# Kernel tuning notes

Hardware: AMD Instinct MI355X
Metric: run time of the kernel (lower is better)

The kernel has to match this reference:

```python
import jax, jax.numpy as jnp
import numpy as np

WS = 32          # window_size (== k passed to rounding helper)
R = 4            # num_relations
H = 8            # num_heads
D = 64           # out_features (head dim)
FIN = 256        # in_features
LENGTHS = [251, 247, 263, 255, 240, 258, 249, 260, 252, 245, 256, 250, 248, 261, 244, 254]


def _statics(lengths, ws):
    """Static index bookkeeping mirroring round_up_to_nearest_k_and_a_window_size,
    insert_zero_rows and the post-hoc index removal in forward()."""
    l = np.asarray(lengths, dtype=np.int64)
    tgt = (l + ws - 1) // ws * ws + ws            # per-graph padded length (+1 extra window)
    starts = np.concatenate([[0], np.cumsum(tgt)[:-1]])
    pad_even = starts - np.arange(len(l)) * ws + l  # padding start in trimmed frame
    pad_odd_win = (starts + tgt - ws) // ws         # window index of each extra padding window
    L = int(tgt.sum())
    w = L // ws
    # positions of real nodes inside the padded sequence
    pos = np.concatenate([s + np.arange(n) for s, n in zip(starts, l)])
    extra = set(pad_odd_win.tolist())
    rem_windows = np.array([i for i in range(w) if i not in extra], dtype=np.int64)
    Wp = len(rem_windows)
    removed = set()
    for p in pad_even:
        nm = (int(p) + ws - 1) // ws * ws
        removed.update(range(int(p), nm))
    rem_final = np.array([i for i in range(Wp * ws) if i not in removed], dtype=np.int64)
    return L, w, pos, rem_windows, rem_final


def setup_inputs() -> dict:
    key = jax.random.key(0)
    k1, k2, k3, k4, k5 = jax.random.split(key, 5)
    N = int(sum(LENGTHS))
    node_features = jax.random.normal(k1, (R, N, FIN), dtype=jnp.float32)
    Wq = jax.random.normal(k2, (H * D, FIN), dtype=jnp.float32) * 0.02
    b_q = jax.random.normal(k3, (H * D,), dtype=jnp.float32) * 0.02
    Wk = jax.random.normal(k4, (H * D, FIN), dtype=jnp.float32) * 0.02
    b_k = jax.random.normal(k5, (H * D,), dtype=jnp.float32) * 0.02
    num_nodes = jnp.asarray(LENGTHS, dtype=jnp.int64)
    return {"node_features": node_features, "Wq": Wq, "b_q": b_q, "Wk": Wk, "b_k": b_k,
            "num_nodes": num_nodes}


def reference(node_features, Wq, b_q, Wk, b_k, num_nodes):
    lengths = np.asarray(num_nodes).tolist()
    L, w, pos, rem_w, rem_f = _statics(lengths, WS)
    Rr, N, Fi = node_features.shape

    # insert_zero_rows: scatter real nodes into padded [R, L, F]; bool key mask [L]
    padded = jnp.zeros((Rr, L, Fi), node_features.dtype).at[:, pos].set(node_features)
    maskL = np.zeros(L, dtype=bool)
    maskL[pos] = True

    # Q/K projections -> [R*H, L, D]
    Q = (padded @ Wq.T + b_q).reshape(Rr, L, H, D).transpose(0, 2, 1, 3).reshape(Rr * H, L, D)
    K = (padded @ Wk.T + b_k).reshape(Rr, L, H, D).transpose(0, 2, 1, 3).reshape(Rr * H, L, D)

    scale = D ** -0.5
    qb = Q.reshape(-1, w, WS, D) * scale            # [B, w, ws, D]
    kb = K.reshape(-1, w, WS, D)
    # look_around keys (backward=1, forward=1, pad_value=-1)
    pk = jnp.pad(kb, ((0, 0), (1, 1), (0, 0), (0, 0)), constant_values=-1.0)
    k3 = jnp.concatenate([pk[:, i:i + w] for i in range(3)], axis=2)  # [B, w, 3ws, D]

    # static validity mask: key-position pad mask AND look-around of real-node mask
    t = np.arange(L).reshape(w, WS)
    pt = np.pad(t, ((1, 1), (0, 0)), constant_values=-1)
    t3 = np.concatenate([pt[i:i + w] for i in range(3)], axis=1)      # [w, 3ws]
    mw = maskL.reshape(w, WS)
    pm = np.pad(mw, ((1, 1), (0, 0)), constant_values=False)
    m3 = np.concatenate([pm[i:i + w] for i in range(3)], axis=1)      # [w, 3ws]
    valid = jnp.asarray(m3 & (t3 != -1))[None, :, None, :]            # [1, w, 1, 3ws]

    sim = jnp.einsum('bwid,bwjd->bwij', qb, k3)                        # [B, w, ws, 3ws]
    NEG = -jnp.finfo(sim.dtype).max
    sim = jnp.where(valid, sim, NEG)

    # drop pure-padding extra windows, softmax (dropout omitted: eval mode)
    attn = jax.nn.softmax(sim[:, rem_w], axis=-1)                      # [B, Wp, ws, 3ws]
    Wp = rem_w.shape[0]
    score = attn.reshape(Rr, H, Wp, WS, 3 * WS).mean(axis=1)           # [R, Wp, ws, 3ws]

    # displace blocks to banded rectangle, then trim first/last window of columns
    wi = np.arange(Wp)[:, None, None]
    ri = np.arange(WS)[None, :, None]
    ci = (np.arange(Wp) * WS)[:, None, None] + np.arange(3 * WS)[None, None, :]
    full = jnp.zeros((Rr, Wp, WS, (Wp + 2) * WS), score.dtype)
    full = full.at[:, wi, ri, ci].set(score)
    rect = full.reshape(Rr, Wp * WS, (Wp + 2) * WS)[:, :, WS:-WS]      # [R, Wp*ws, Wp*ws]

    # remove intra-window padding rows and columns
    rect = rect[:, rem_f][:, :, rem_f]                                 # [R, N, N]
    n = rem_f.shape[0]
    return rect.transpose(1, 0, 2).reshape(n, Rr * n)                  # [N, R*N]
```

## Files before the change

### kernel.cpp

```cpp
#include <hip/hip_runtime.h>
#include <stdint.h>

typedef float f32x4 __attribute__((ext_vector_type(4)));
typedef short s16x8 __attribute__((ext_vector_type(8)));
typedef unsigned short u16x4 __attribute__((ext_vector_type(4)));
typedef unsigned short u16x8 __attribute__((ext_vector_type(8)));

#define NG 16
__constant__ int c_LEN[NG]   = {251,247,263,255,240,258,249,260,252,245,256,250,248,261,244,254};
__constant__ int c_CUM[NG+1] = {0,251,498,761,1016,1256,1514,1763,2023,2275,2520,2776,3026,3274,3535,3779,4033};
__constant__ int c_KWC[NG+1] = {0,8,16,25,33,41,50,58,67,75,83,91,99,107,116,124,132};

#define NTOT 4033
#define RN   16132
#define NWIN 132
#define NEGF (-3.0e38f)

#define ZS 2304
#define ZCHUNKA 9292032L
#define ZBLOCKS 2024
#define AZB 264

#define OFF_WB 8259584
#define OFF_QK 8783872

__device__ __forceinline__ unsigned short f2bf(float f){
  union { float f; uint32_t u; } x; x.f = f;
  uint32_t u = x.u;
  u += 0x7fffu + ((u >> 16) & 1u);
  return (unsigned short)(u >> 16);
}

__device__ __forceinline__ f32x4 mfma16(s16x8 a, s16x8 b, f32x4 c){
  return __builtin_amdgcn_mfma_f32_16x16x32_bf16(a, b, c, 0, 0, 0);
}

#define NX4  1032448
#define NWQ4 32768
#define NCV4 1097984
__global__ void convert_kernel(const float* __restrict__ X,
                               const float* __restrict__ Wq,
                               const float* __restrict__ Wk,
                               unsigned short* __restrict__ Xb,
                               unsigned short* __restrict__ Wb){
  int i = blockIdx.x * 256 + threadIdx.x;
  if (i >= NCV4) return;
  const float* src; unsigned short* dst;
  if (i < NX4){ src = X + (size_t)i * 4; dst = Xb + (size_t)i * 4; }
  else {
    int k = i - NX4;
    if (k < NWQ4){ src = Wq + (size_t)k * 4; dst = Wb + (size_t)k * 4; }
    else         { src = Wk + (size_t)(k - NWQ4) * 4; dst = Wb + (size_t)k * 4; }
  }
  f32x4 v = *(const f32x4*)src;
  u16x4 o;
  #pragma unroll
  for (int c = 0; c < 4; ++c) o[c] = f2bf(v[c]);
  *(u16x4*)dst = o;
}

#define LP 68
__global__ __launch_bounds__(256) void projzero_kernel(const unsigned short* __restrict__ Xb,
                                                       const unsigned short* __restrict__ Wb,
                                                       const float* __restrict__ bq,
                                                       const float* __restrict__ bk,
                                                       unsigned short* __restrict__ QK,
                                                       float* __restrict__ out){
  __shared__ float tile[64 * LP];

  int bid = blockIdx.x;
  int grp = bid / 3;
  int rem = bid - grp * 3;

  if (rem == 2){
    f32x4 z = {0.f, 0.f, 0.f, 0.f};
    f32x4* o4 = (f32x4*)out;
    long stride = (long)ZBLOCKS * 256;
    for (long i = (long)grp * 256 + threadIdx.x; i < ZCHUNKA; i += stride)
      o4[i] = z;
    return;
  }

  int pi = grp * 2 + rem;
  int col0 = (pi & 15) * 64;
  int row0 = (pi >> 4) * 64;

  int tid  = threadIdx.x;
  int lane = tid & 63, wid = tid >> 6;
  int l15  = lane & 15, quad = lane >> 4;
  int wm = wid & 1, wn = wid >> 1;
  int rowW = row0 + wm * 32;
  int colW = col0 + wn * 32;

  f32x4 acc[2][2];
  #pragma unroll
  for (int m = 0; m < 2; ++m)
    #pragma unroll
    for (int n = 0; n < 2; ++n){ acc[m][n][0]=0.f; acc[m][n][1]=0.f; acc[m][n][2]=0.f; acc[m][n][3]=0.f; }

  int r0 = min(rowW + l15,      RN - 1);
  int r1 = min(rowW + 16 + l15, RN - 1);
  const unsigned short* a0p = Xb + (size_t)r0 * 256 + quad * 8;
  const unsigned short* a1p = Xb + (size_t)r1 * 256 + quad * 8;
  const unsigned short* b0p = Wb + (size_t)(colW + l15)      * 256 + quad * 8;
  const unsigned short* b1p = Wb + (size_t)(colW + 16 + l15) * 256 + quad * 8;

  #pragma unroll
  for (int k = 0; k < 256; k += 32){
    s16x8 a0 = *(const s16x8*)(a0p + k);
    s16x8 a1 = *(const s16x8*)(a1p + k);
    s16x8 b0 = *(const s16x8*)(b0p + k);
    s16x8 b1 = *(const s16x8*)(b1p + k);
    acc[0][0] = mfma16(a0, b0, acc[0][0]);
    acc[0][1] = mfma16(a0, b1, acc[0][1]);
    acc[1][0] = mfma16(a1, b0, acc[1][0]);
    acc[1][1] = mfma16(a1, b1, acc[1][1]);
  }

  #pragma unroll
  for (int m = 0; m < 2; ++m)
  #pragma unroll
  for (int n = 0; n < 2; ++n)
  #pragma unroll
  for (int g = 0; g < 4; ++g){
    int rL = wm * 32 + m * 16 + quad * 4 + g;
    int cL = wn * 32 + n * 16 + l15;
    tile[rL * LP + cL] = acc[m][n][g];
  }
  __syncthreads();

  int rL = tid >> 2;
  int cB = (tid & 3) * 16;
  int row = row0 + rL;
  if (row < RN){
    int col = col0 + cB;
    const float* bias = (col < 512) ? (bq + col) : (bk + col - 512);
    float sc = (col < 512) ? 0.125f : 1.0f;
    u16x8 o0, o1;
    #pragma unroll
    for (int i = 0; i < 8; ++i)
      o0[i] = f2bf((tile[rL * LP + cB + i] + bias[i]) * sc);
    #pragma unroll
    for (int i = 0; i < 8; ++i)
      o1[i] = f2bf((tile[rL * LP + cB + 8 + i] + bias[8 + i]) * sc);
    *(u16x8*)(QK + (size_t)row * 1024 + col)     = o0;
    *(u16x8*)(QK + (size_t)row * 1024 + col + 8) = o1;
  }
}

__global__ __launch_bounds__(512, 4) void attnzero_kernel(const unsigned short* __restrict__ QK,
                                                          float* __restrict__ out){
  __shared__ float part[4][32 * 97];

  int bid = blockIdx.x;
  int grp = bid / 3;
  int rem = bid - grp * 3;

  if (rem == 2){
    for (int row = ZS + grp; row < NTOT; row += AZB){
      int g = 0;
      #pragma unroll
      for (int i = 0; i < NG; ++i) if (row >= c_CUM[i + 1]) g = i + 1;
      int base = c_CUM[g], l = c_LEN[g];
      int lw = (row - base) >> 5;
      int kb = base + max(0, (lw << 5) - 32);
      int ke = base + min(l, (lw << 5) + 64);
      float* orow = out + (size_t)row * RN;
      for (int c = threadIdx.x; c < 4033; c += 512){
        int col0 = c << 2;
        int r0 = (col0 >= 12099) ? 3 : (col0 >= 8066) ? 2 : (col0 >= 4033) ? 1 : 0;
        int col3 = col0 + 3;
        int r3 = (col3 >= 12099) ? 3 : (col3 >= 8066) ? 2 : (col3 >= 4033) ? 1 : 0;
        if (r0 == r3){
          int cr = col0 - r0 * NTOT;
          if (cr + 4 <= kb || cr >= ke){
            f32x4 z = {0.f, 0.f, 0.f, 0.f};
            *(f32x4*)(orow + col0) = z;
          } else if (cr >= kb && cr + 4 <= ke){
          } else {
            #pragma unroll
            for (int i = 0; i < 4; ++i){
              int cc = cr + i;
              if (cc < kb || cc >= ke) orow[col0 + i] = 0.f;
            }
          }
        } else {
          #pragma unroll
          for (int i = 0; i < 4; ++i){
            int col = col0 + i;
            int r = (col >= 12099) ? 3 : (col >= 8066) ? 2 : (col >= 4033) ? 1 : 0;
            int cr = col - r * NTOT;
            if (cr < kb || cr >= ke) orow[col] = 0.f;
          }
        }
      }
    }
    return;
  }

  int b  = grp * 2 + rem;
  int r  = b / NWIN;
  int wq = b % NWIN;
  int g = 0;
  #pragma unroll
  for (int i = 0; i < NG; ++i) if (wq >= c_KWC[i + 1]) g = i + 1;
  int lw   = wq - c_KWC[g];
  int l    = c_LEN[g];
  int base = c_CUM[g];
  int qbeg = lw * 32;
  int qnum = min(32, l - qbeg);
  int kbeg = max(0, qbeg - 32);
  int kend = min(l, qbeg + 64);
  int knum = kend - kbeg;

  int tid  = threadIdx.x;
  int lane = tid & 63, wid = tid >> 6;
  int l15  = lane & 15, quad = lane >> 4;
  int rbase = r * NTOT + base;
  int h = wid;

  bool valid[6];
  #pragma unroll
  for (int n = 0; n < 6; ++n) valid[n] = (n * 16 + l15) < knum;

  s16x8 qf[2][2];
  #pragma unroll
  for (int m = 0; m < 2; ++m){
    int qi = min(qbeg + m * 16 + l15, l - 1);
    const unsigned short* qp = QK + (size_t)(rbase + qi) * 1024 + h * 64 + quad * 8;
    qf[m][0] = *(const s16x8*)qp;
    qf[m][1] = *(const s16x8*)(qp + 32);
  }
  f32x4 s[2][6];
  #pragma unroll
  for (int n = 0; n < 6; ++n){
    int ki = min(kbeg + n * 16 + l15, l - 1);
    const unsigned short* kp = QK + (size_t)(rbase + ki) * 1024 + 512 + h * 64 + quad * 8;
    s16x8 kf0 = *(const s16x8*)kp;
    s16x8 kf1 = *(const s16x8*)(kp + 32);
    #pragma unroll
    for (int m = 0; m < 2; ++m){
      f32x4 z; z[0]=0.f; z[1]=0.f; z[2]=0.f; z[3]=0.f;
      z = mfma16(qf[m][0], kf0, z);
      s[m][n] = mfma16(qf[m][1], kf1, z);
    }
  }
  #pragma unroll
  for (int m = 0; m < 2; ++m)
    #pragma unroll
    for (int n = 0; n < 6; ++n)
      if (!valid[n]){ s[m][n][0]=NEGF; s[m][n][1]=NEGF; s[m][n][2]=NEGF; s[m][n][3]=NEGF; }

  #pragma unroll
  for (int m = 0; m < 2; ++m){
    f32x4 mx = s[m][0];
    #pragma unroll
    for (int n = 1; n < 6; ++n)
      #pragma unroll
      for (int c = 0; c < 4; ++c) mx[c] = fmaxf(mx[c], s[m][n][c]);
    #pragma unroll
    for (int c = 0; c < 4; ++c){
      float v = mx[c];
      v = fmaxf(v, __shfl_xor(v, 1));
      v = fmaxf(v, __shfl_xor(v, 2));
      v = fmaxf(v, __shfl_xor(v, 4));
      v = fmaxf(v, __shfl_xor(v, 8));
      mx[c] = v;
    }
    f32x4 sum; sum[0]=0.f; sum[1]=0.f; sum[2]=0.f; sum[3]=0.f;
    #pragma unroll
    for (int n = 0; n < 6; ++n)
      #pragma unroll
      for (int c = 0; c < 4; ++c){
        float e = __expf(s[m][n][c] - mx[c]);
        s[m][n][c] = e;
        sum[c] += e;
      }
    #pragma unroll
    for (int c = 0; c < 4; ++c){
      float v = sum[c];
      v += __shfl_xor(v, 1);
      v += __shfl_xor(v, 2);
      v += __shfl_xor(v, 4);
      v += __shfl_xor(v, 8);
      sum[c] = v;
    }
    f32x4 scv;
    #pragma unroll
    for (int c = 0; c < 4; ++c) scv[c] = 0.125f / sum[c];
    #pragma unroll
    for (int n = 0; n < 6; ++n)
      #pragma unroll
      for (int c = 0; c < 4; ++c) s[m][n][c] *= scv[c];
  }

  if (wid >= 4){
    #pragma unroll
    for (int m = 0; m < 2; ++m)
    #pragma unroll
    for (int n = 0; n < 6; ++n)
    #pragma unroll
    for (int c = 0; c < 4; ++c){
      int row = m * 16 + quad * 4 + c;
      int col = n * 16 + l15;
      part[wid - 4][row * 97 + col] = s[m][n][c];
    }
  }
  __syncthreads();
  if (wid < 4){
    #pragma unroll
    for (int m = 0; m < 2; ++m)
    #pragma unroll
    for (int n = 0; n < 6; ++n)
    #pragma unroll
    for (int c = 0; c < 4; ++c){
      int row = m * 16 + quad * 4 + c;
      int col = n * 16 + l15;
      part[wid][row * 97 + col] += s[m][n][c];
    }
  }
  __syncthreads();

  for (int e = tid; e < 32 * 96; e += 512){
    int row = e / 96, col = e % 96;
    if (row < qnum && col < knum){
      float v = part[0][row * 97 + col] + part[1][row * 97 + col]
              + part[2][row * 97 + col] + part[3][row * 97 + col];
      long nq = base + qbeg + row;
      long mk = base + kbeg + col;
      out[nq * (long)RN + (long)r * NTOT + mk] = v;
    }
  }
}

extern "C" void kernel_launch(void* const* d_in, const int* in_sizes, int n_in,
                              void* d_out, int out_size, void* d_ws, size_t ws_size,
                              hipStream_t stream){
  const float* X  = (const float*)d_in[0];
  const float* Wq = (const float*)d_in[1];
  const float* bq = (const float*)d_in[2];
  const float* Wk = (const float*)d_in[3];
  const float* bk = (const float*)d_in[4];
  float* out = (float*)d_out;

  char* ws = (char*)d_ws;
  unsigned short* Xb = (unsigned short*)ws;
  unsigned short* Wb = (unsigned short*)(ws + OFF_WB);
  unsigned short* QK = (unsigned short*)(ws + OFF_QK);

  convert_kernel<<<(NCV4 + 255) / 256, 256, 0, stream>>>(X, Wq, Wk, Xb, Wb);
  projzero_kernel<<<3 * ZBLOCKS, 256, 0, stream>>>(Xb, Wb, bq, bk, QK, out);
  attnzero_kernel<<<3 * AZB, 512, 0, stream>>>(QK, out);
}
```

Before: 357.2 us.

## Fuse X bf16 conversion into projection kernel and rebalance output zeroing

Drops the separate pass that converted all of X to bf16 and instead converts each 64-row tile into shared memory inside the projection kernel. Each block keeps its A fragments in registers and loops over all 16 column tiles, so X is read once per row tile instead of once per column tile. Output zero-fill is moved into dedicated trailing blocks that cover rows up to 2000, with the attention kernel zeroing the remaining rows, and the zero stores are made nontemporal. The projection now runs on only 253 blocks, each doing 16x the work, which may reduce MFMA parallelism and overlap with the zeroing. The launch-bounds occupancy hint on the attention kernel is also removed.

```diff
diff --git a/kernel.cpp b/kernel.cpp
--- a/kernel.cpp
+++ b/kernel.cpp
@@ -16,13 +16,13 @@
 #define NWIN 132
 #define NEGF (-3.0e38f)
 
-#define ZS 2304
-#define ZCHUNKA 9292032L
-#define ZBLOCKS 2024
-#define AZB 264
-
-#define OFF_WB 8259584
-#define OFF_QK 8783872
+#define ZROW   2000
+#define Z2CH   8066000L
+#define PBLK   253
+#define ZB2    1518
+#define AZB    264
+
+#define OFF_QK 524288
 
 __device__ __forceinline__ unsigned short f2bf(float f){
   union { float f; uint32_t u; } x; x.f = f;
@@ -35,129 +35,133 @@
   return __builtin_amdgcn_mfma_f32_16x16x32_bf16(a, b, c, 0, 0, 0);
 }
 
-#define NX4  1032448
-#define NWQ4 32768
-#define NCV4 1097984
-__global__ void convert_kernel(const float* __restrict__ X,
-                               const float* __restrict__ Wq,
-                               const float* __restrict__ Wk,
-                               unsigned short* __restrict__ Xb,
-                               unsigned short* __restrict__ Wb){
-  int i = blockIdx.x * 256 + threadIdx.x;
-  if (i >= NCV4) return;
-  const float* src; unsigned short* dst;
-  if (i < NX4){ src = X + (size_t)i * 4; dst = Xb + (size_t)i * 4; }
-  else {
-    int k = i - NX4;
-    if (k < NWQ4){ src = Wq + (size_t)k * 4; dst = Wb + (size_t)k * 4; }
-    else         { src = Wk + (size_t)(k - NWQ4) * 4; dst = Wb + (size_t)k * 4; }
-  }
-  f32x4 v = *(const f32x4*)src;
-  u16x4 o;
-  #pragma unroll
-  for (int c = 0; c < 4; ++c) o[c] = f2bf(v[c]);
-  *(u16x4*)dst = o;
+#define WCH 65536
+__global__ __launch_bounds__(256) void wcvt_kernel(const float* __restrict__ Wq,
+                                                   const float* __restrict__ Wk,
+                                                   unsigned short* __restrict__ Wb){
+  for (int j = blockIdx.x * 256 + threadIdx.x; j < WCH; j += 64 * 256){
+    const float* src = (j < WCH/2) ? (Wq + (size_t)j * 4)
+                                   : (Wk + (size_t)(j - WCH/2) * 4);
+    f32x4 v = *(const f32x4*)src;
+    u16x4 o;
+    #pragma unroll
+    for (int c = 0; c < 4; ++c) o[c] = f2bf(v[c]);
+    *(u16x4*)(Wb + (size_t)j * 4) = o;
+  }
 }
 
 #define LP 68
-__global__ __launch_bounds__(256) void projzero_kernel(const unsigned short* __restrict__ Xb,
+__global__ __launch_bounds__(256) void projzero_kernel(const float* __restrict__ X,
                                                        const unsigned short* __restrict__ Wb,
                                                        const float* __restrict__ bq,
                                                        const float* __restrict__ bk,
                                                        unsigned short* __restrict__ QK,
                                                        float* __restrict__ out){
-  __shared__ float tile[64 * LP];
+  __shared__ char smem[64 * 264 * 2];
+  unsigned short* xs = (unsigned short*)smem;
+  float* tile = (float*)smem;
+
+  int bid = blockIdx.x;
+  if (bid >= PBLK){
+    int grp = bid - PBLK;
+    f32x4 z = {0.f, 0.f, 0.f, 0.f};
+    f32x4* o4 = (f32x4*)out;
+    long stride = (long)ZB2 * 256;
+    for (long i = (long)grp * 256 + threadIdx.x; i < Z2CH; i += stride)
+      __builtin_nontemporal_store(z, o4 + i);
+    return;
+  }
+
+  int tid  = threadIdx.x;
+  int row0 = bid * 64;
+
+  for (int c = tid; c < 4096; c += 256){
+    int rr = c >> 6, c4 = c & 63;
+    int gr = min(row0 + rr, RN - 1);
+    f32x4 v = *(const f32x4*)(X + (size_t)gr * 256 + c4 * 4);
+    u16x4 o;
+    #pragma unroll
+    for (int i = 0; i < 4; ++i) o[i] = f2bf(v[i]);
+    *(u16x4*)(xs + rr * 264 + c4 * 4) = o;
+  }
+  __syncthreads();
+
+  int lane = tid & 63, wid = tid >> 6;
+  int l15  = lane & 15, quad = lane >> 4;
+  int wm = wid & 1, wn = wid >> 1;
+
+  s16x8 aR[2][8];
+  #pragma unroll
+  for (int m = 0; m < 2; ++m)
+    #pragma unroll
+    for (int kk = 0; kk < 8; ++kk)
+      aR[m][kk] = *(const s16x8*)(xs + (wm * 32 + m * 16 + l15) * 264 + kk * 32 + quad * 8);
+
+  for (int ct = 0; ct < 16; ++ct){
+    int col0 = ct * 64;
+    int colW = col0 + wn * 32;
+    const unsigned short* b0p = Wb + (size_t)(colW + l15)      * 256 + quad * 8;
+    const unsigned short* b1p = Wb + (size_t)(colW + 16 + l15) * 256 + quad * 8;
+
+    f32x4 acc[2][2];
+    #pragma unroll
+    for (int m = 0; m < 2; ++m)
+      #pragma unroll
+      for (int n = 0; n < 2; ++n){ acc[m][n][0]=0.f; acc[m][n][1]=0.f; acc[m][n][2]=0.f; acc[m][n][3]=0.f; }
+
+    #pragma unroll
+    for (int kk = 0; kk < 8; ++kk){
+      s16x8 b0 = *(const s16x8*)(b0p + kk * 32);
+      s16x8 b1 = *(const s16x8*)(b1p + kk * 32);
+      acc[0][0] = mfma16(aR[0][kk], b0, acc[0][0]);
+      acc[0][1] = mfma16(aR[0][kk], b1, acc[0][1]);
+      acc[1][0] = mfma16(aR[1][kk], b0, acc[1][0]);
+      acc[1][1] = mfma16(aR[1][kk], b1, acc[1][1]);
+    }
+
+    __syncthreads();
+    #pragma unroll
+    for (int m = 0; m < 2; ++m)
+    #pragma unroll
+    for (int n = 0; n < 2; ++n)
+    #pragma unroll
+    for (int g = 0; g < 4; ++g){
+      int rL = wm * 32 + m * 16 + quad * 4 + g;
+      int cL = wn * 32 + n * 16 + l15;
+      tile[rL * LP + cL] = acc[m][n][g];
+    }
+    __syncthreads();
+
+    int rL = tid >> 2;
+    int cB = (tid & 3) * 16;
+    int row = row0 + rL;
+    if (row < RN){
+      int col = col0 + cB;
+      const float* bias = (col < 512) ? (bq + col) : (bk + col - 512);
+      float sc = (col < 512) ? 0.125f : 1.0f;
+      u16x8 o0, o1;
+      #pragma unroll
+      for (int i = 0; i < 8; ++i)
+        o0[i] = f2bf((tile[rL * LP + cB + i] + bias[i]) * sc);
+      #pragma unroll
+      for (int i = 0; i < 8; ++i)
+        o1[i] = f2bf((tile[rL * LP + cB + 8 + i] + bias[8 + i]) * sc);
+      *(u16x8*)(QK + (size_t)row * 1024 + col)     = o0;
+      *(u16x8*)(QK + (size_t)row * 1024 + col + 8) = o1;
+    }
+  }
+}
+
+__global__ __launch_bounds__(512) void attnzero_kernel(const unsigned short* __restrict__ QK,
+                                                       float* __restrict__ out){
+  __shared__ float part[4][32 * 97];
 
   int bid = blockIdx.x;
   int grp = bid / 3;
   int rem = bid - grp * 3;
 
   if (rem == 2){
-    f32x4 z = {0.f, 0.f, 0.f, 0.f};
-    f32x4* o4 = (f32x4*)out;
-    long stride = (long)ZBLOCKS * 256;
-    for (long i = (long)grp * 256 + threadIdx.x; i < ZCHUNKA; i += stride)
-      o4[i] = z;
-    return;
-  }
-
-  int pi = grp * 2 + rem;
-  int col0 = (pi & 15) * 64;
-  int row0 = (pi >> 4) * 64;
-
-  int tid  = threadIdx.x;
-  int lane = tid & 63, wid = tid >> 6;
-  int l15  = lane & 15, quad = lane >> 4;
-  int wm = wid & 1, wn = wid >> 1;
-  int rowW = row0 + wm * 32;
-  int colW = col0 + wn * 32;
-
-  f32x4 acc[2][2];
-  #pragma unroll
-  for (int m = 0; m < 2; ++m)
-    #pragma unroll
-    for (int n = 0; n < 2; ++n){ acc[m][n][0]=0.f; acc[m][n][1]=0.f; acc[m][n][2]=0.f; acc[m][n][3]=0.f; }
-
-  int r0 = min(rowW + l15,      RN - 1);
-  int r1 = min(rowW + 16 + l15, RN - 1);
-  const unsigned short* a0p = Xb + (size_t)r0 * 256 + quad * 8;
-  const unsigned short* a1p = Xb + (size_t)r1 * 256 + quad * 8;
-  const unsigned short* b0p = Wb + (size_t)(colW + l15)      * 256 + quad * 8;
-  const unsigned short* b1p = Wb + (size_t)(colW + 16 + l15) * 256 + quad * 8;
-
-  #pragma unroll
-  for (int k = 0; k < 256; k += 32){
-    s16x8 a0 = *(const s16x8*)(a0p + k);
-    s16x8 a1 = *(const s16x8*)(a1p + k);
-    s16x8 b0 = *(const s16x8*)(b0p + k);
-    s16x8 b1 = *(const s16x8*)(b1p + k);
-    acc[0][0] = mfma16(a0, b0, acc[0][0]);
-    acc[0][1] = mfma16(a0, b1, acc[0][1]);
-    acc[1][0] = mfma16(a1, b0, acc[1][0]);
-    acc[1][1] = mfma16(a1, b1, acc[1][1]);
-  }
-
-  #pragma unroll
-  for (int m = 0; m < 2; ++m)
-  #pragma unroll
-  for (int n = 0; n < 2; ++n)
-  #pragma unroll
-  for (int g = 0; g < 4; ++g){
-    int rL = wm * 32 + m * 16 + quad * 4 + g;
-    int cL = wn * 32 + n * 16 + l15;
-    tile[rL * LP + cL] = acc[m][n][g];
-  }
-  __syncthreads();
-
-  int rL = tid >> 2;
-  int cB = (tid & 3) * 16;
-  int row = row0 + rL;
-  if (row < RN){
-    int col = col0 + cB;
-    const float* bias = (col < 512) ? (bq + col) : (bk + col - 512);
-    float sc = (col < 512) ? 0.125f : 1.0f;
-    u16x8 o0, o1;
-    #pragma unroll
-    for (int i = 0; i < 8; ++i)
-      o0[i] = f2bf((tile[rL * LP + cB + i] + bias[i]) * sc);
-    #pragma unroll
-    for (int i = 0; i < 8; ++i)
-      o1[i] = f2bf((tile[rL * LP + cB + 8 + i] + bias[8 + i]) * sc);
-    *(u16x8*)(QK + (size_t)row * 1024 + col)     = o0;
-    *(u16x8*)(QK + (size_t)row * 1024 + col + 8) = o1;
-  }
-}
-
-__global__ __launch_bounds__(512, 4) void attnzero_kernel(const unsigned short* __restrict__ QK,
-                                                          float* __restrict__ out){
-  __shared__ float part[4][32 * 97];
-
-  int bid = blockIdx.x;
-  int grp = bid / 3;
-  int rem = bid - grp * 3;
-
-  if (rem == 2){
-    for (int row = ZS + grp; row < NTOT; row += AZB){
+    for (int row = ZROW + grp; row < NTOT; row += AZB){
       int g = 0;
       #pragma unroll
       for (int i = 0; i < NG; ++i) if (row >= c_CUM[i + 1]) g = i + 1;
@@ -175,7 +179,7 @@
           int cr = col0 - r0 * NTOT;
           if (cr + 4 <= kb || cr >= ke){
             f32x4 z = {0.f, 0.f, 0.f, 0.f};
-            *(f32x4*)(orow + col0) = z;
+            __builtin_nontemporal_store(z, (f32x4*)(orow + col0));
           } else if (cr >= kb && cr + 4 <= ke){
           } else {
             #pragma unroll
@@ -344,11 +348,10 @@
   float* out = (float*)d_out;
 
   char* ws = (char*)d_ws;
-  unsigned short* Xb = (unsigned short*)ws;
-  unsigned short* Wb = (unsigned short*)(ws + OFF_WB);
+  unsigned short* Wb = (unsigned short*)ws;
   unsigned short* QK = (unsigned short*)(ws + OFF_QK);
 
-  convert_kernel<<<(NCV4 + 255) / 256, 256, 0, stream>>>(X, Wq, Wk, Xb, Wb);
-  projzero_kernel<<<3 * ZBLOCKS, 256, 0, stream>>>(Xb, Wb, bq, bk, QK, out);
+  wcvt_kernel<<<64, 256, 0, stream>>>(Wq, Wk, Wb);
+  projzero_kernel<<<PBLK + ZB2, 256, 0, stream>>>(X, Wb, bq, bk, QK, out);
   attnzero_kernel<<<3 * AZB, 512, 0, stream>>>(QK, out);
 }
```

After: 361.4 us. About the same (+1.2%).
